# Performance work log

Hardware: AMD Instinct MI355X
Metric: run time of the kernel (lower is better)

## Reference

```python
import jax, jax.numpy as jnp
import numpy as np

NUM_TREE = 64
TREE_DEPTH = 4
NUM_LEAF = 2 ** (TREE_DEPTH + 1)        # 32
NUM_INTERNALS = NUM_LEAF - 1            # 31
IN_DIM = 512
OUT_DIM = 16
BATCH = 8192


def build_route_masks(tree_depth: int, num_internals: int, num_leaf: int) -> np.ndarray:
    """Static gather indices into the [p, 1-p] concatenated prob vector (length 2*num_internals).
    Returns [tree_depth+1, num_leaf]; product over level axis gives leaf path probabilities.
    Mirrors the increment_mask construction in the torch forward."""
    masks = []
    num_repeat = num_leaf // 2
    num_local_internals = 1
    masks.append(np.repeat(np.array([0, num_internals]), num_repeat))
    for _ in range(1, tree_depth + 1):
        num_repeat //= 2
        num_local_internals *= 2
        m = np.repeat(np.arange(num_local_internals - 1, 2 * num_local_internals - 1), 2)
        m = m + np.tile(np.array([0, num_internals]), num_local_internals)
        m = np.repeat(m, num_repeat)
        masks.append(m)
    return np.stack(masks).astype(np.int32)  # [depth+1, num_leaf]


ROUTE_MASKS = jnp.asarray(build_route_masks(TREE_DEPTH, NUM_INTERNALS, NUM_LEAF))


def setup_inputs() -> dict:
    key = jax.random.key(0)
    k1, k2, k3 = jax.random.split(key, 3)
    x = jax.random.normal(k1, (BATCH, IN_DIM), dtype=jnp.float32)
    # xavier-ish scale so sigmoid gates are not saturated
    W = jax.random.normal(k2, (NUM_TREE * NUM_INTERNALS, IN_DIM), dtype=jnp.float32) / np.sqrt(IN_DIM)
    b = jnp.zeros((NUM_TREE * NUM_INTERNALS,), dtype=jnp.float32)
    leafs = jax.random.normal(k3, (NUM_TREE, NUM_LEAF, OUT_DIM), dtype=jnp.float32)
    return {"x": x, "W": W, "b": b, "leafs": leafs}


def reference(x, W, b, leafs) -> jnp.ndarray:
    B = x.shape[0]
    T, L, O = leafs.shape
    I = L - 1
    tree_net = x @ W.T + b                                  # [B, T*I]
    p = jax.nn.sigmoid(tree_net).reshape(B, T, I)           # split per tree
    flat = jnp.concatenate([p, 1.0 - p], axis=-1)           # [B, T, 2I]
    gathered = flat[:, :, ROUTE_MASKS]                      # [B, T, depth+1, L]
    routes = jnp.prod(gathered, axis=2)                     # [B, T, L] leaf path probs
    leafs_sm = jax.nn.softmax(leafs, axis=-1)
    features = routes.reshape(B, T * L)
    out = features @ leafs_sm.reshape(T * L, O) / T
    return out
```

## Files before the change

### kernel.cpp

```cpp
#include <hip/hip_runtime.h>

#define BATCH 8192
#define IN_DIM 512
#define NT 64
#define NI 31
#define NL 32
#define ODIM 16
#define NPAD (NT*NL)
#define NCB 16

typedef __attribute__((ext_vector_type(8))) short bf16x8;
typedef __attribute__((ext_vector_type(4))) float f32x4;

__device__ __forceinline__ unsigned short f2b(float f) {
  union { float f; unsigned int u; } v; v.f = f;
  unsigned int r = v.u + 0x7fffu + ((v.u >> 16) & 1u);
  return (unsigned short)(r >> 16);
}
__device__ __forceinline__ float b2f(unsigned short h) {
  union { unsigned int u; float f; } v; v.u = ((unsigned int)h) << 16;
  return v.f;
}

__global__ __launch_bounds__(256) void prep_kernel(
    const float* __restrict__ x, const float* __restrict__ W,
    const float* __restrict__ leafs,
    unsigned short* __restrict__ xb, unsigned short* __restrict__ wb,
    float* __restrict__ lsm)
{
  const int NXg = BATCH * (IN_DIM/8);
  const int NWg = NPAD  * (IN_DIM/8);
  const int NS  = NT*NL;
  int gid = blockIdx.x*256 + threadIdx.x;
  if (gid < NXg) {
    int row = gid >> 6, k8 = gid & 63;
    int kt = k8 >> 2, g = k8 & 3;
    int gs = g ^ ((row >> 1) & 3);
    const float* s = x + (size_t)row*IN_DIM + kt*32 + gs*8;
    float4 v0 = ((const float4*)s)[0], v1 = ((const float4*)s)[1];
    ushort4 o0, o1;
    o0.x=f2b(v0.x); o0.y=f2b(v0.y); o0.z=f2b(v0.z); o0.w=f2b(v0.w);
    o1.x=f2b(v1.x); o1.y=f2b(v1.y); o1.z=f2b(v1.z); o1.w=f2b(v1.w);
    ((ushort4*)xb)[gid*2]   = o0;
    ((ushort4*)xb)[gid*2+1] = o1;
  } else if ((gid -= NXg) < NWg) {
    int row = gid >> 6, k8 = gid & 63;
    int t = row >> 5, i = row & 31;
    int kt = k8 >> 2, g = k8 & 3;
    int gs = g ^ ((row >> 1) & 3);
    ushort4 o0, o1;
    if (i == 31) { o0.x=o0.y=o0.z=o0.w=0; o1=o0; }
    else {
      const float* s = W + (size_t)(t*NI+i)*IN_DIM + kt*32 + gs*8;
      float4 v0 = ((const float4*)s)[0], v1 = ((const float4*)s)[1];
      o0.x=f2b(v0.x); o0.y=f2b(v0.y); o0.z=f2b(v0.z); o0.w=f2b(v0.w);
      o1.x=f2b(v1.x); o1.y=f2b(v1.y); o1.z=f2b(v1.z); o1.w=f2b(v1.w);
    }
    ((ushort4*)wb)[gid*2]   = o0;
    ((ushort4*)wb)[gid*2+1] = o1;
  } else if ((gid -= NWg) < NS) {
    const float* src = leafs + (size_t)gid*ODIM;
    float m = src[0];
    #pragma unroll
    for (int o=1;o<ODIM;++o) m = fmaxf(m, src[o]);
    float e[ODIM]; float s = 0.f;
    #pragma unroll
    for (int o=0;o<ODIM;++o) { e[o] = __expf(src[o]-m); s += e[o]; }
    float inv = 1.f/(s*(float)NT);
    #pragma unroll
    for (int o=0;o<ODIM;++o) lsm[(size_t)gid*ODIM+o] = e[o]*inv;
  }
}

__device__ __forceinline__ void async16(const unsigned short* g, unsigned short* l) {
  __builtin_amdgcn_global_load_lds(
      (const __attribute__((address_space(1))) unsigned int*)g,
      (__attribute__((address_space(3))) unsigned int*)l,
      16, 0, 0);
}

#define STG 8192

__global__ __launch_bounds__(256, 4) void fused_kernel(
    const unsigned short* __restrict__ xb, const unsigned short* __restrict__ wb,
    const float* __restrict__ bias, const float* __restrict__ lsm,
    float* __restrict__ part)
{
  __shared__ __align__(16) unsigned short smem[17408];

  const int tid  = threadIdx.x;
  const int lane = tid & 63;
  const int wave = tid >> 6;
  const int wm = wave & 1, wn = wave >> 1;

  const int bid  = blockIdx.x;
  const int loc  = bid >> 3;
  const int n_t  = loc & 15;
  const int m_t  = (bid & 7)*8 + (loc >> 4);
  const int m0 = m_t * 128, n0 = n_t * 128;

  f32x4 acc[4][4];
  #pragma unroll
  for (int i=0;i<4;++i)
    #pragma unroll
    for (int j=0;j<4;++j) { f32x4 z = {0.f,0.f,0.f,0.f}; acc[i][j] = z; }

  const int srow = lane >> 2, scol = (lane & 3) * 8;
  const int qa = wave*2;
  const unsigned short* ga0 = xb + (size_t)(m0 + qa*16 + srow)*IN_DIM + scol;
  const unsigned short* gb0 = wb + (size_t)(n0 + qa*16 + srow)*IN_DIM + scol;

  const int l15 = lane & 15, quad = lane >> 4;
  const int cs   = (quad ^ ((l15 >> 1) & 3)) << 3;

  async16(ga0,             smem + qa*512);
  async16(ga0 + 16*IN_DIM, smem + qa*512 + 512);
  async16(gb0,             smem + 4096 + qa*512);
  async16(gb0 + 16*IN_DIM, smem + 4096 + qa*512 + 512);

  for (int kt = 0; kt < 16; ++kt) {
    __syncthreads();
    const int cur = (kt & 1) * STG;
    if (kt < 15) {
      const int nxt = ((kt + 1) & 1) * STG;
      const int ko = (kt + 1) * 32;
      async16(ga0 + ko,             smem + nxt + qa*512);
      async16(ga0 + ko + 16*IN_DIM, smem + nxt + qa*512 + 512);
      async16(gb0 + ko,             smem + nxt + 4096 + qa*512);
      async16(gb0 + ko + 16*IN_DIM, smem + nxt + 4096 + qa*512 + 512);
    }
    const unsigned short* As = smem + cur;
    const unsigned short* Bs = smem + cur + 4096;
    bf16x8 af[4], bfr[4];
    #pragma unroll
    for (int mi=0;mi<4;++mi)
      af[mi] = *(const bf16x8*)(As + (wm*64 + mi*16 + l15)*32 + cs);
    #pragma unroll
    for (int ni=0;ni<4;++ni)
      bfr[ni] = *(const bf16x8*)(Bs + (wn*64 + ni*16 + l15)*32 + cs);
    #pragma unroll
    for (int mi=0;mi<4;++mi)
      #pragma unroll
      for (int ni=0;ni<4;++ni)
        acc[mi][ni] = __builtin_amdgcn_mfma_f32_16x16x32_bf16(
            af[mi], bfr[ni], acc[mi][ni], 0, 0, 0);
  }

  bf16x8 bleaf[4];
  {
    const int t0 = n_t * 4;
    #pragma unroll
    for (int s=0;s<4;++s) {
      union { bf16x8 v; unsigned short u[8]; } tmp;
      #pragma unroll
      for (int j=0;j<8;++j)
        tmp.u[j] = f2b(lsm[((size_t)(t0+s)*NL + quad*8 + j)*ODIM + l15]);
      bleaf[s] = tmp.v;
    }
  }

  __syncthreads();

  unsigned short* Pt = smem;
  #pragma unroll
  for (int ni=0;ni<4;++ni) {
    int cl = wn*64 + ni*16 + l15;
    int gcol = n0 + cl;
    int tt = gcol >> 5, ii = gcol & 31;
    float bv = (ii < NI) ? bias[tt*NI + ii] : 0.f;
    #pragma unroll
    for (int mi=0;mi<4;++mi) {
      int lrow = wm*64 + mi*16 + quad*4;
      #pragma unroll
      for (int r=0;r<4;++r) {
        float v = acc[mi][ni][r] + bv;
        Pt[(lrow + r)*130 + cl] = f2b(1.f/(1.f + __expf(-v)));
      }
    }
  }
  __syncthreads();

  const int row  = tid >> 1;
  const int half = tid & 1;
  unsigned int rt[32];
  #pragma unroll
  for (int sel=0; sel<2; ++sel) {
    const int tl = half*2 + sel;
    const unsigned short* pr = Pt + row*130 + tl*32;
    float v[32];
    float p0 = b2f(pr[0]);
    v[0] = p0; v[1] = 1.f - p0;
    #pragma unroll
    for (int d=1; d<=4; ++d) {
      const int s = 1 << d;
      #pragma unroll
      for (int j=s-1; j>=0; --j) {
        float pj = b2f(pr[(s-1)+j]);
        float base = v[j];
        v[2*j]   = base * pj;
        v[2*j+1] = base * (1.f - pj);
      }
    }
    #pragma unroll
    for (int k=0;k<16;++k)
      rt[sel*16+k] = (unsigned int)f2b(v[2*k]) | ((unsigned int)f2b(v[2*k+1]) << 16);
  }
  __syncthreads();

  unsigned int* Rt32 = (unsigned int*)smem;
  {
    uint4* dst = (uint4*)(Rt32 + row*68 + half*32);
    #pragma unroll
    for (int c=0;c<8;++c) {
      uint4 w; w.x=rt[c*4]; w.y=rt[c*4+1]; w.z=rt[c*4+2]; w.w=rt[c*4+3];
      dst[c] = w;
    }
  }
  __syncthreads();

  const unsigned short* RtS = smem;
  #pragma unroll
  for (int mt=0; mt<2; ++mt) {
    const int mrow = (wave*2 + mt)*16;
    f32x4 a2 = {0.f,0.f,0.f,0.f};
    #pragma unroll
    for (int s=0;s<4;++s) {
      bf16x8 af2 = *(const bf16x8*)(RtS + (mrow + l15)*136 + s*32 + quad*8);
      a2 = __builtin_amdgcn_mfma_f32_16x16x32_bf16(af2, bleaf[s], a2, 0, 0, 0);
    }
    float* op = part + ((size_t)n_t*BATCH + (m0 + mrow + quad*4))*ODIM + l15;
    #pragma unroll
    for (int r=0;r<4;++r)
      op[r*ODIM] = a2[r];
  }
}

__global__ __launch_bounds__(256) void reduce_kernel(
    const float* __restrict__ part, float* __restrict__ out)
{
  int gid = blockIdx.x*256 + threadIdx.x;
  const float4* p4 = (const float4*)part;
  float4 s = p4[gid];
  #pragma unroll
  for (int cb=1; cb<NCB; ++cb) {
    float4 v = p4[(size_t)cb*(BATCH*ODIM/4) + gid];
    s.x+=v.x; s.y+=v.y; s.z+=v.z; s.w+=v.w;
  }
  ((float4*)out)[gid] = s;
}

extern "C" void kernel_launch(void* const* d_in, const int* in_sizes, int n_in,
                              void* d_out, int out_size, void* d_ws, size_t ws_size,
                              hipStream_t stream) {
  const float* x     = (const float*)d_in[0];
  const float* W     = (const float*)d_in[1];
  const float* b     = (const float*)d_in[2];
  const float* leafs = (const float*)d_in[3];
  float* out = (float*)d_out;

  char* ws = (char*)d_ws;
  unsigned short* xb  = (unsigned short*)ws;
  unsigned short* wb  = (unsigned short*)(ws + 8388608);
  float*          lsm = (float*)(ws + 10485760);
  float*          part= (float*)(ws + 10616832);

  const int total = BATCH*(IN_DIM/8) + NPAD*(IN_DIM/8) + NT*NL;
  prep_kernel<<<dim3((total + 255)/256), dim3(256), 0, stream>>>(
      x, W, leafs, xb, wb, lsm);
  fused_kernel<<<dim3(1024), dim3(256), 0, stream>>>(
      xb, wb, b, lsm, part);
  reduce_kernel<<<dim3(BATCH*ODIM/4/256), dim3(256), 0, stream>>>(part, out);
}
```

Baseline: 104.9 us.

## Pre-pack operands in MFMA fragment order and load directly into registers

The prep kernel now writes x and W in bf16, packed in 16-row strips in the exact per-lane fragment order the MFMA expects. The GEMM main loop then loads each fragment straight from global memory into registers, with no LDS staging, async copies or per-step barriers, and the launch bound drops to 3 waves. This removes LDS traffic and synchronisation in the K loop. In exchange, each wave reads its operands from global/L2 with no sharing between waves inside the block, and register pressure goes up.

```diff
diff --git a/kernel.cpp b/kernel.cpp
--- a/kernel.cpp
+++ b/kernel.cpp
@@ -25,34 +25,36 @@
 __global__ __launch_bounds__(256) void prep_kernel(
     const float* __restrict__ x, const float* __restrict__ W,
     const float* __restrict__ leafs,
-    unsigned short* __restrict__ xb, unsigned short* __restrict__ wb,
+    unsigned short* __restrict__ xa, unsigned short* __restrict__ wb,
     float* __restrict__ lsm)
 {
-  const int NXg = BATCH * (IN_DIM/8);
-  const int NWg = NPAD  * (IN_DIM/8);
+  const int NXg = BATCH*IN_DIM/8;
+  const int NWg = NPAD*IN_DIM/8;
   const int NS  = NT*NL;
   int gid = blockIdx.x*256 + threadIdx.x;
   if (gid < NXg) {
-    int row = gid >> 6, k8 = gid & 63;
-    int kt = k8 >> 2, g = k8 & 3;
-    int gs = g ^ ((row >> 1) & 3);
-    const float* s = x + (size_t)row*IN_DIM + kt*32 + gs*8;
-    float4 v0 = ((const float4*)s)[0], v1 = ((const float4*)s)[1];
+    int strip = gid >> 10, rem = gid & 1023;
+    int w = rem >> 6, rem2 = rem & 63;
+    int quad = rem2 >> 4, c = rem2 & 15;
+    int m = strip*16 + c;
+    const float4* s = (const float4*)(x + (size_t)m*IN_DIM + w*32 + quad*8);
+    float4 v0 = s[0], v1 = s[1];
     ushort4 o0, o1;
     o0.x=f2b(v0.x); o0.y=f2b(v0.y); o0.z=f2b(v0.z); o0.w=f2b(v0.w);
     o1.x=f2b(v1.x); o1.y=f2b(v1.y); o1.z=f2b(v1.z); o1.w=f2b(v1.w);
-    ((ushort4*)xb)[gid*2]   = o0;
-    ((ushort4*)xb)[gid*2+1] = o1;
+    ((ushort4*)xa)[gid*2]   = o0;
+    ((ushort4*)xa)[gid*2+1] = o1;
   } else if ((gid -= NXg) < NWg) {
-    int row = gid >> 6, k8 = gid & 63;
-    int t = row >> 5, i = row & 31;
-    int kt = k8 >> 2, g = k8 & 3;
-    int gs = g ^ ((row >> 1) & 3);
+    int strip = gid >> 10, rem = gid & 1023;
+    int w = rem >> 6, rem2 = rem & 63;
+    int quad = rem2 >> 4, c = rem2 & 15;
+    int n = strip*16 + c;
+    int t = n >> 5, i = n & 31;
     ushort4 o0, o1;
     if (i == 31) { o0.x=o0.y=o0.z=o0.w=0; o1=o0; }
     else {
-      const float* s = W + (size_t)(t*NI+i)*IN_DIM + kt*32 + gs*8;
-      float4 v0 = ((const float4*)s)[0], v1 = ((const float4*)s)[1];
+      const float4* s = (const float4*)(W + (size_t)(t*NI+i)*IN_DIM + w*32 + quad*8);
+      float4 v0 = s[0], v1 = s[1];
       o0.x=f2b(v0.x); o0.y=f2b(v0.y); o0.z=f2b(v0.z); o0.w=f2b(v0.w);
       o1.x=f2b(v1.x); o1.y=f2b(v1.y); o1.z=f2b(v1.z); o1.w=f2b(v1.w);
     }
@@ -72,17 +74,8 @@
   }
 }
 
-__device__ __forceinline__ void async16(const unsigned short* g, unsigned short* l) {
-  __builtin_amdgcn_global_load_lds(
-      (const __attribute__((address_space(1))) unsigned int*)g,
-      (__attribute__((address_space(3))) unsigned int*)l,
-      16, 0, 0);
-}
-
-#define STG 8192
-
-__global__ __launch_bounds__(256, 4) void fused_kernel(
-    const unsigned short* __restrict__ xb, const unsigned short* __restrict__ wb,
+__global__ __launch_bounds__(256, 3) void fused_kernel(
+    const unsigned short* __restrict__ xa, const unsigned short* __restrict__ wb,
     const float* __restrict__ bias, const float* __restrict__ lsm,
     float* __restrict__ part)
 {
@@ -105,39 +98,20 @@
     #pragma unroll
     for (int j=0;j<4;++j) { f32x4 z = {0.f,0.f,0.f,0.f}; acc[i][j] = z; }
 
-  const int srow = lane >> 2, scol = (lane & 3) * 8;
-  const int qa = wave*2;
-  const unsigned short* ga0 = xb + (size_t)(m0 + qa*16 + srow)*IN_DIM + scol;
-  const unsigned short* gb0 = wb + (size_t)(n0 + qa*16 + srow)*IN_DIM + scol;
-
   const int l15 = lane & 15, quad = lane >> 4;
-  const int cs   = (quad ^ ((l15 >> 1) & 3)) << 3;
-
-  async16(ga0,             smem + qa*512);
-  async16(ga0 + 16*IN_DIM, smem + qa*512 + 512);
-  async16(gb0,             smem + 4096 + qa*512);
-  async16(gb0 + 16*IN_DIM, smem + 4096 + qa*512 + 512);
-
-  for (int kt = 0; kt < 16; ++kt) {
-    __syncthreads();
-    const int cur = (kt & 1) * STG;
-    if (kt < 15) {
-      const int nxt = ((kt + 1) & 1) * STG;
-      const int ko = (kt + 1) * 32;
-      async16(ga0 + ko,             smem + nxt + qa*512);
-      async16(ga0 + ko + 16*IN_DIM, smem + nxt + qa*512 + 512);
-      async16(gb0 + ko,             smem + nxt + 4096 + qa*512);
-      async16(gb0 + ko + 16*IN_DIM, smem + nxt + 4096 + qa*512 + 512);
-    }
-    const unsigned short* As = smem + cur;
-    const unsigned short* Bs = smem + cur + 4096;
+
+  const unsigned short* pA = xa + ((size_t)(m_t*8 + wm*4))*8192 + lane*8;
+  const unsigned short* pB = wb + ((size_t)(n_t*8 + wn*4))*8192 + lane*8;
+
+  #pragma unroll
+  for (int w = 0; w < 16; ++w) {
     bf16x8 af[4], bfr[4];
     #pragma unroll
     for (int mi=0;mi<4;++mi)
-      af[mi] = *(const bf16x8*)(As + (wm*64 + mi*16 + l15)*32 + cs);
+      af[mi]  = *(const bf16x8*)(pA + mi*8192 + w*512);
     #pragma unroll
     for (int ni=0;ni<4;++ni)
-      bfr[ni] = *(const bf16x8*)(Bs + (wn*64 + ni*16 + l15)*32 + cs);
+      bfr[ni] = *(const bf16x8*)(pB + ni*8192 + w*512);
     #pragma unroll
     for (int mi=0;mi<4;++mi)
       #pragma unroll
@@ -158,8 +132,6 @@
       bleaf[s] = tmp.v;
     }
   }
-
-  __syncthreads();
 
   unsigned short* Pt = smem;
   #pragma unroll
@@ -259,15 +231,15 @@
   float* out = (float*)d_out;
 
   char* ws = (char*)d_ws;
-  unsigned short* xb  = (unsigned short*)ws;
+  unsigned short* xa  = (unsigned short*)ws;
   unsigned short* wb  = (unsigned short*)(ws + 8388608);
   float*          lsm = (float*)(ws + 10485760);
   float*          part= (float*)(ws + 10616832);
 
   const int total = BATCH*(IN_DIM/8) + NPAD*(IN_DIM/8) + NT*NL;
   prep_kernel<<<dim3((total + 255)/256), dim3(256), 0, stream>>>(
-      x, W, leafs, xb, wb, lsm);
+      x, W, leafs, xa, wb, lsm);
   fused_kernel<<<dim3(1024), dim3(256), 0, stream>>>(
-      xb, wb, b, lsm, part);
+      xa, wb, b, lsm, part);
   reduce_kernel<<<dim3(BATCH*ODIM/4/256), dim3(256), 0, stream>>>(part, out);
 }
```

Result: slower. 117.1 us (+11.6%).
